# Optimization experiments

Hardware: AMD Instinct MI355X
Metric: run time of the kernel (lower is better)

The kernel has to match this reference:

```python
import jax, jax.numpy as jnp
import numpy as np

N_HEADS = 12
EMBED_DIM = 768
QKV_DIM = 64


def setup_inputs() -> dict:
    key = jax.random.key(0)
    ks = jax.random.split(key, 6)
    x = jax.random.normal(ks[0], (32, 577, EMBED_DIM), dtype=jnp.float32)
    # per-head Linear weights, torch layout [out, in] stacked over heads: [H, D, E]
    s = 1.0 / np.sqrt(EMBED_DIM)
    wq = jax.random.uniform(ks[1], (N_HEADS, QKV_DIM, EMBED_DIM), jnp.float32, -s, s)
    wk = jax.random.uniform(ks[2], (N_HEADS, QKV_DIM, EMBED_DIM), jnp.float32, -s, s)
    wv = jax.random.uniform(ks[3], (N_HEADS, QKV_DIM, EMBED_DIM), jnp.float32, -s, s)
    sp = 1.0 / np.sqrt(N_HEADS * QKV_DIM)
    w_proj = jax.random.uniform(ks[4], (EMBED_DIM, N_HEADS * QKV_DIM), jnp.float32, -sp, sp)
    b_proj = jax.random.uniform(ks[5], (EMBED_DIM,), jnp.float32, -sp, sp)
    return {"x": x, "wq": wq, "wk": wk, "wv": wv, "w_proj": w_proj, "b_proj": b_proj}


def reference(x, wq, wk, wv, w_proj, b_proj):
    scale = QKV_DIM ** (-0.5)
    # batched per-head projections: x [B,S,E], w* [H,D,E] -> [B,H,S,D]
    q = jnp.einsum('bse,hde->bhsd', x, wq)
    k = jnp.einsum('bse,hde->bhsd', x, wk)
    v = jnp.einsum('bse,hde->bhsd', x, wv)
    scores = jnp.einsum('bhsd,bhtd->bhst', q, k) * scale  # [B,H,S,S]
    attn = jax.nn.softmax(scores, axis=-1)
    out = jnp.einsum('bhst,bhtd->bhsd', attn, v)          # [B,H,S,D]
    # concat heads in head order along last dim: [B,S,H*D]
    B, H, S, D = out.shape
    cat = jnp.transpose(out, (0, 2, 1, 3)).reshape(B, S, H * D)
    return cat @ w_proj.T + b_proj
```

## Files before the change

### kernel.cpp

```cpp
#include <hip/hip_runtime.h>

#define TOK    18464
#define SEQ    577
#define EMB    768
#define NH     12
#define HD     64
#define HEADSZ 36928
#define PLANE  14180352
#define SPAD   640

typedef float f32x4 __attribute__((ext_vector_type(4)));
typedef short s16x8 __attribute__((ext_vector_type(8)));

__device__ __forceinline__ unsigned short f2bf(float f) {
  unsigned u = __builtin_bit_cast(unsigned, f);
  return (unsigned short)((u + 0x7fffu + ((u >> 16) & 1u)) >> 16);
}
__device__ __forceinline__ unsigned pk2bf(float a, float b) {
  return (unsigned)f2bf(a) | ((unsigned)f2bf(b) << 16);
}
__device__ __forceinline__ float fexp2(float x) {
  float r; asm("v_exp_f32 %0, %1" : "=v"(r) : "v"(x)); return r;
}

__device__ __forceinline__ void gload16(const void* g, void* l) {
  __builtin_amdgcn_global_load_lds(
      (const __attribute__((address_space(1))) void*)g,
      (__attribute__((address_space(3))) void*)l, 16, 0, 0);
}

__global__ void cvt_x(const float* __restrict__ src, short* __restrict__ dst, int n8) {
  int i = blockIdx.x * blockDim.x + threadIdx.x;
  if (i >= n8) return;
  const float4* s4 = reinterpret_cast<const float4*>(src + (size_t)i * 8);
  float4 a = s4[0], b = s4[1];
  s16x8 o;
  o[0] = (short)f2bf(a.x); o[1] = (short)f2bf(a.y);
  o[2] = (short)f2bf(a.z); o[3] = (short)f2bf(a.w);
  o[4] = (short)f2bf(b.x); o[5] = (short)f2bf(b.y);
  o[6] = (short)f2bf(b.z); o[7] = (short)f2bf(b.w);
  *reinterpret_cast<s16x8*>(dst + (size_t)i * 8) = o;
}

__global__ void cvt_w(const float* __restrict__ wq, const float* __restrict__ wk,
                      const float* __restrict__ wv, const float* __restrict__ wp,
                      short* __restrict__ wqkv, short* __restrict__ wpb) {
  int tid = blockIdx.x * blockDim.x + threadIdx.x;
  if (tid >= 294912) return;
  int region = tid / 73728;
  int off = (tid % 73728) * 8;
  const float* s; short* d;
  if (region == 0)      { s = wq + off; d = wqkv + off; }
  else if (region == 1) { s = wk + off; d = wqkv + 589824 + off; }
  else if (region == 2) { s = wv + off; d = wqkv + 2 * 589824 + off; }
  else                  { s = wp + off; d = wpb + off; }
  const float4* s4 = reinterpret_cast<const float4*>(s);
  float4 a = s4[0], b = s4[1];
  s16x8 o;
  o[0] = (short)f2bf(a.x); o[1] = (short)f2bf(a.y);
  o[2] = (short)f2bf(a.z); o[3] = (short)f2bf(a.w);
  o[4] = (short)f2bf(b.x); o[5] = (short)f2bf(b.y);
  o[6] = (short)f2bf(b.z); o[7] = (short)f2bf(b.w);
  *reinterpret_cast<s16x8*>(d) = o;
}

template <int MODE>
__launch_bounds__(256)
__global__ void gemm_bt(const short* __restrict__ A, const short* __restrict__ Bw,
                        short* __restrict__ qk_out, short* __restrict__ vt_out,
                        float* __restrict__ out, const float* __restrict__ bias,
                        int M, int nnt) {
  __shared__ short As[128 * 32];
  __shared__ short Bs[128 * 32];
  int bid = blockIdx.x, nwg = gridDim.x;
  int qq = nwg >> 3, rr = nwg & 7;
  int xcd = bid & 7, loc = bid >> 3;
  int wgid = (xcd < rr ? xcd * (qq + 1) : rr * (qq + 1) + (xcd - rr) * qq) + loc;
  int tn = wgid % nnt;
  int tm = wgid / nnt;
  int tid = threadIdx.x;
  int w = tid >> 6, lane = tid & 63;
  int wm = w >> 1, wn = w & 1;
  int lr = lane & 15, lg = lane >> 4;
  int m0 = tm * 128, n0 = tn * 128;

  f32x4 acc[4][4] = {};

  int srow = tid >> 2;
  int scol = (tid & 3) * 8;

  for (int kt = 0; kt < 24; ++kt) {
    int kb = kt * 32;
    __syncthreads();
    #pragma unroll
    for (int it = 0; it < 2; ++it) {
      int row = srow + it * 64;
      int gr = m0 + row; if (gr >= M) gr = M - 1;
      gload16(A + (size_t)gr * EMB + kb + scol, (char*)As + w * 1024 + it * 4096);
      int rb = n0 + row;
      gload16(Bw + (size_t)rb * EMB + kb + scol, (char*)Bs + w * 1024 + it * 4096);
    }
    __syncthreads();
    s16x8 af[4], bfr[4];
    #pragma unroll
    for (int f = 0; f < 4; ++f) {
      af[f]  = *reinterpret_cast<const s16x8*>(&As[(wm * 64 + f * 16 + lr) * 32 + lg * 8]);
      bfr[f] = *reinterpret_cast<const s16x8*>(&Bs[(wn * 64 + f * 16 + lr) * 32 + lg * 8]);
    }
    #pragma unroll
    for (int i = 0; i < 4; ++i)
      #pragma unroll
      for (int j = 0; j < 4; ++j)
        acc[i][j] = __builtin_amdgcn_mfma_f32_16x16x32_bf16(af[i], bfr[j], acc[i][j], 0, 0, 0);
  }

  int mbase = m0 + wm * 64;
  int nbase = n0 + wn * 64;
  #pragma unroll
  for (int i = 0; i < 4; ++i) {
    #pragma unroll
    for (int j = 0; j < 4; ++j) {
      #pragma unroll
      for (int r = 0; r < 4; ++r) {
        int row = mbase + i * 16 + lg * 4 + r;
        int col = nbase + j * 16 + lr;
        if (row < M) {
          float v = acc[i][j][r];
          if (MODE == 0) {
            int b = row / SEQ;
            int s = row - b * SEQ;
            if (col >= 1536) {
              int rem = col - 1536;
              int h = rem >> 6, d = rem & 63;
              vt_out[((size_t)(b * NH + h) * HD + d) * SPAD + s] = (short)f2bf(v);
            } else {
              int which = (col >= 768) ? 1 : 0;
              int rem = col - which * 768;
              int h = rem >> 6, d = rem & 63;
              qk_out[(size_t)which * PLANE + ((size_t)b * NH + h) * HEADSZ + s * HD + d] =
                  (short)f2bf(v);
            }
          } else {
            out[(size_t)row * EMB + col] = v + bias[col];
          }
        }
      }
    }
  }
}

__launch_bounds__(256)
__global__ void attn(const short* __restrict__ qkv, const short* __restrict__ vt,
                     short* __restrict__ cat) {
  int bid = blockIdx.x;
  int wgid = (bid & 7) * 240 + (bid >> 3);
  int bh = wgid / 5, qt = wgid % 5;
  int b = bh / NH, h = bh % NH;
  const short* Q   = qkv + (size_t)bh * HEADSZ;
  const char* KpB  = (const char*)(qkv + (size_t)PLANE + (size_t)bh * HEADSZ);
  const char* VtpB = (const char*)(vt + (size_t)bh * (HD * SPAD));

  __shared__ char KVs[16384];
  __shared__ short Pl[4][32 * 72];

  int tid = threadIdx.x, w = tid >> 6, lane = tid & 63;
  int lr = lane & 15, lg = lane >> 4;
  int q0 = qt * 128;
  short* Pw = &Pl[w][0];

  s16x8 qf[2][2];
  #pragma unroll
  for (int rb = 0; rb < 2; ++rb) {
    int row = q0 + w * 32 + rb * 16 + lr; if (row >= SEQ) row = SEQ - 1;
    #pragma unroll
    for (int kk = 0; kk < 2; ++kk)
      qf[rb][kk] = *reinterpret_cast<const s16x8*>(&Q[row * HD + kk * 32 + lg * 8]);
  }

  int srow0 = tid >> 3;
  int scb   = (tid & 7) * 16;
  int swz  = (lr & 7) << 4;
  int ka0  = lr * 128 + ((lg * 16) ^ swz);

  f32x4 acco[2][4] = {};
  float lsum[2] = {0.f, 0.f};
  const float SCL = 0.18033688f;
  const f32x4 NEG16 = {-16.f, -16.f, -16.f, -16.f};

  for (int tt = 0; tt < 10; ++tt) {
    int t0 = tt * 64;

    __syncthreads();
    #pragma unroll
    for (int it = 0; it < 2; ++it) {
      int row = srow0 + it * 32;
      int cb  = scb ^ ((row & 7) << 4);
      int ldst = row * 128 + scb;
      int grow = t0 + row; if (grow > 576) grow = 576;
      gload16(KpB + (size_t)grow * 128 + cb, KVs + ldst);
      gload16(VtpB + (size_t)row * (SPAD * 2) + t0 * 2 + cb, KVs + 8192 + ldst);
    }
    __syncthreads();

    #pragma unroll
    for (int fk = 0; fk < 4; ++fk) {
      s16x8 kf0 = *reinterpret_cast<const s16x8*>(KVs + fk * 2048 + ka0);
      s16x8 kf1 = *reinterpret_cast<const s16x8*>(KVs + fk * 2048 + (ka0 ^ 64));
      f32x4 s0 = NEG16, s1 = NEG16;
      s0 = __builtin_amdgcn_mfma_f32_16x16x32_bf16(kf0, qf[0][0], s0, 0, 0, 0);
      s0 = __builtin_amdgcn_mfma_f32_16x16x32_bf16(kf1, qf[0][1], s0, 0, 0, 0);
      s1 = __builtin_amdgcn_mfma_f32_16x16x32_bf16(kf0, qf[1][0], s1, 0, 0, 0);
      s1 = __builtin_amdgcn_mfma_f32_16x16x32_bf16(kf1, qf[1][1], s1, 0, 0, 0);
      #pragma unroll
      for (int r = 0; r < 4; ++r) {
        bool ok = (t0 + fk * 16 + lg * 4 + r) < SEQ;
        s0[r] = ok ? s0[r] * SCL : -1e30f;
        s1[r] = ok ? s1[r] * SCL : -1e30f;
      }
      {
        float p0 = fexp2(s0[0]), p1 = fexp2(s0[1]);
        float p2 = fexp2(s0[2]), p3 = fexp2(s0[3]);
        lsum[0] += (p0 + p1) + (p2 + p3);
        uint2 pk; pk.x = pk2bf(p0, p1); pk.y = pk2bf(p2, p3);
        *reinterpret_cast<uint2*>(&Pw[(size_t)lr * 72 + fk * 16 + lg * 4]) = pk;
      }
      {
        float p0 = fexp2(s1[0]), p1 = fexp2(s1[1]);
        float p2 = fexp2(s1[2]), p3 = fexp2(s1[3]);
        lsum[1] += (p0 + p1) + (p2 + p3);
        uint2 pk; pk.x = pk2bf(p0, p1); pk.y = pk2bf(p2, p3);
        *reinterpret_cast<uint2*>(&Pw[(size_t)(16 + lr) * 72 + fk * 16 + lg * 4]) = pk;
      }
    }

    s16x8 pf[2][2];
    #pragma unroll
    for (int rb = 0; rb < 2; ++rb)
      #pragma unroll
      for (int kk = 0; kk < 2; ++kk)
        pf[rb][kk] = *reinterpret_cast<const s16x8*>(&Pw[(rb * 16 + lr) * 72 + kk * 32 + lg * 8]);

    #pragma unroll
    for (int f = 0; f < 4; ++f) {
      s16x8 vf0 = *reinterpret_cast<const s16x8*>(KVs + 8192 + f * 2048 + ka0);
      s16x8 vf1 = *reinterpret_cast<const s16x8*>(KVs + 8192 + f * 2048 + (ka0 ^ 64));
      acco[0][f] = __builtin_amdgcn_mfma_f32_16x16x32_bf16(pf[0][0], vf0, acco[0][f], 0, 0, 0);
      acco[0][f] = __builtin_amdgcn_mfma_f32_16x16x32_bf16(pf[0][1], vf1, acco[0][f], 0, 0, 0);
      acco[1][f] = __builtin_amdgcn_mfma_f32_16x16x32_bf16(pf[1][0], vf0, acco[1][f], 0, 0, 0);
      acco[1][f] = __builtin_amdgcn_mfma_f32_16x16x32_bf16(pf[1][1], vf1, acco[1][f], 0, 0, 0);
    }
  }

  #pragma unroll
  for (int rb = 0; rb < 2; ++rb) {
    lsum[rb] += __shfl_xor(lsum[rb], 16);
    lsum[rb] += __shfl_xor(lsum[rb], 32);
  }

  #pragma unroll
  for (int rb = 0; rb < 2; ++rb) {
    #pragma unroll
    for (int r = 0; r < 4; ++r) {
      float li = __shfl(lsum[rb], lg * 4 + r);
      int s = q0 + w * 32 + rb * 16 + lg * 4 + r;
      if (s < SEQ) {
        float inv = 1.0f / li;
        #pragma unroll
        for (int f = 0; f < 4; ++f)
          cat[((size_t)b * SEQ + s) * EMB + h * HD + f * 16 + lr] =
              (short)f2bf(acco[rb][f][r] * inv);
      }
    }
  }
}

extern "C" void kernel_launch(void* const* d_in, const int* in_sizes, int n_in,
                              void* d_out, int out_size, void* d_ws, size_t ws_size,
                              hipStream_t stream) {
  const float* x  = (const float*)d_in[0];
  const float* wq = (const float*)d_in[1];
  const float* wk = (const float*)d_in[2];
  const float* wv = (const float*)d_in[3];
  const float* wp = (const float*)d_in[4];
  const float* bp = (const float*)d_in[5];
  float* out = (float*)d_out;

  char* ws = (char*)d_ws;
  short* xb   = (short*)ws;
  short* wqkv = (short*)(ws + 28360704);
  short* wpb  = (short*)(ws + 31899648);
  short* qkb  = (short*)(ws + 33079296);
  short* vtb  = (short*)(ws + 89800704);
  short* cat  = xb;

  hipMemsetAsync(vtb, 0, 31457280, stream);
  cvt_x<<<6924, 256, 0, stream>>>(x, xb, 1772544);
  cvt_w<<<1152, 256, 0, stream>>>(wq, wk, wv, wp, wqkv, wpb);
  gemm_bt<0><<<145 * 18, 256, 0, stream>>>(xb, wqkv, qkb, vtb, nullptr, nullptr, TOK, 18);
  attn<<<1920, 256, 0, stream>>>(qkb, vtb, cat);
  gemm_bt<1><<<145 * 6, 256, 0, stream>>>(cat, wpb, nullptr, nullptr, out, bp, TOK, 6);
}
```

Baseline: 273.1 us.

## Double-buffer LDS tiles in GEMM and attention to overlap loads with MFMA

Adds two-stage LDS double buffering to both the bf16 GEMM and the attention kernel. The next K-slice (or K/V tile) is prefetched into the alternate buffer with direct-to-LDS loads while MFMAs run on the current one, and each iteration now needs one barrier instead of two. The goal is to hide global load latency. In exchange LDS use doubles (32 KB for the GEMM, about 50 KB for attention), which may reduce occupancy. Correctness relies on gload16 completing before the trailing barrier, so the change depends on the compiler inserting the right vmcnt waits.

```diff
diff --git a/kernel.cpp b/kernel.cpp
--- a/kernel.cpp
+++ b/kernel.cpp
@@ -70,8 +70,8 @@
                         short* __restrict__ qk_out, short* __restrict__ vt_out,
                         float* __restrict__ out, const float* __restrict__ bias,
                         int M, int nnt) {
-  __shared__ short As[128 * 32];
-  __shared__ short Bs[128 * 32];
+  __shared__ short As[2][128 * 32];
+  __shared__ short Bs[2][128 * 32];
   int bid = blockIdx.x, nwg = gridDim.x;
   int qq = nwg >> 3, rr = nwg & 7;
   int xcd = bid & 7, loc = bid >> 3;
@@ -89,30 +89,41 @@
   int srow = tid >> 2;
   int scol = (tid & 3) * 8;
 
+#define G_STAGE(buf, kt)                                                          \
+  {                                                                               \
+    int kb = (kt) * 32;                                                           \
+    _Pragma("unroll")                                                             \
+    for (int it = 0; it < 2; ++it) {                                              \
+      int row = srow + it * 64;                                                   \
+      int gr = m0 + row; if (gr >= M) gr = M - 1;                                 \
+      gload16(A + (size_t)gr * EMB + kb + scol, (char*)As[buf] + w * 1024 + it * 4096); \
+      int rb = n0 + row;                                                          \
+      gload16(Bw + (size_t)rb * EMB + kb + scol, (char*)Bs[buf] + w * 1024 + it * 4096); \
+    }                                                                             \
+  }
+
+  G_STAGE(0, 0);
+  __syncthreads();
+
   for (int kt = 0; kt < 24; ++kt) {
-    int kb = kt * 32;
-    __syncthreads();
-    #pragma unroll
-    for (int it = 0; it < 2; ++it) {
-      int row = srow + it * 64;
-      int gr = m0 + row; if (gr >= M) gr = M - 1;
-      gload16(A + (size_t)gr * EMB + kb + scol, (char*)As + w * 1024 + it * 4096);
-      int rb = n0 + row;
-      gload16(Bw + (size_t)rb * EMB + kb + scol, (char*)Bs + w * 1024 + it * 4096);
-    }
-    __syncthreads();
+    int cur = kt & 1;
+    if (kt < 23) G_STAGE(cur ^ 1, kt + 1);
+
     s16x8 af[4], bfr[4];
     #pragma unroll
     for (int f = 0; f < 4; ++f) {
-      af[f]  = *reinterpret_cast<const s16x8*>(&As[(wm * 64 + f * 16 + lr) * 32 + lg * 8]);
-      bfr[f] = *reinterpret_cast<const s16x8*>(&Bs[(wn * 64 + f * 16 + lr) * 32 + lg * 8]);
+      af[f]  = *reinterpret_cast<const s16x8*>(&As[cur][(wm * 64 + f * 16 + lr) * 32 + lg * 8]);
+      bfr[f] = *reinterpret_cast<const s16x8*>(&Bs[cur][(wn * 64 + f * 16 + lr) * 32 + lg * 8]);
     }
     #pragma unroll
     for (int i = 0; i < 4; ++i)
       #pragma unroll
       for (int j = 0; j < 4; ++j)
         acc[i][j] = __builtin_amdgcn_mfma_f32_16x16x32_bf16(af[i], bfr[j], acc[i][j], 0, 0, 0);
-  }
+
+    __syncthreads();
+  }
+#undef G_STAGE
 
   int mbase = m0 + wm * 64;
   int nbase = n0 + wn * 64;
@@ -160,7 +171,7 @@
   const char* KpB  = (const char*)(qkv + (size_t)PLANE + (size_t)bh * HEADSZ);
   const char* VtpB = (const char*)(vt + (size_t)bh * (HD * SPAD));
 
-  __shared__ char KVs[16384];
+  __shared__ char KVs[2][16384];
   __shared__ short Pl[4][32 * 72];
 
   int tid = threadIdx.x, w = tid >> 6, lane = tid & 63;
@@ -187,25 +198,34 @@
   const float SCL = 0.18033688f;
   const f32x4 NEG16 = {-16.f, -16.f, -16.f, -16.f};
 
+#define KV_STAGE(buf, t0s)                                                        \
+  {                                                                               \
+    _Pragma("unroll")                                                             \
+    for (int it = 0; it < 2; ++it) {                                              \
+      int row = srow0 + it * 32;                                                  \
+      int cb  = scb ^ ((row & 7) << 4);                                           \
+      int ldst = row * 128 + scb;                                                 \
+      int grow = (t0s) + row; if (grow > 576) grow = 576;                         \
+      gload16(KpB + (size_t)grow * 128 + cb, KVs[buf] + ldst);                    \
+      gload16(VtpB + (size_t)row * (SPAD * 2) + (t0s) * 2 + cb, KVs[buf] + 8192 + ldst); \
+    }                                                                             \
+  }
+
+  KV_STAGE(0, 0);
+  __syncthreads();
+
   for (int tt = 0; tt < 10; ++tt) {
     int t0 = tt * 64;
-
-    __syncthreads();
-    #pragma unroll
-    for (int it = 0; it < 2; ++it) {
-      int row = srow0 + it * 32;
-      int cb  = scb ^ ((row & 7) << 4);
-      int ldst = row * 128 + scb;
-      int grow = t0 + row; if (grow > 576) grow = 576;
-      gload16(KpB + (size_t)grow * 128 + cb, KVs + ldst);
-      gload16(VtpB + (size_t)row * (SPAD * 2) + t0 * 2 + cb, KVs + 8192 + ldst);
-    }
-    __syncthreads();
+    int cur = tt & 1;
+    if (tt < 9) KV_STAGE(cur ^ 1, t0 + 64);
+
+    const char* Ks = KVs[cur];
+    const char* Vs = KVs[cur] + 8192;
 
     #pragma unroll
     for (int fk = 0; fk < 4; ++fk) {
-      s16x8 kf0 = *reinterpret_cast<const s16x8*>(KVs + fk * 2048 + ka0);
-      s16x8 kf1 = *reinterpret_cast<const s16x8*>(KVs + fk * 2048 + (ka0 ^ 64));
+      s16x8 kf0 = *reinterpret_cast<const s16x8*>(Ks + fk * 2048 + ka0);
+      s16x8 kf1 = *reinterpret_cast<const s16x8*>(Ks + fk * 2048 + (ka0 ^ 64));
       f32x4 s0 = NEG16, s1 = NEG16;
       s0 = __builtin_amdgcn_mfma_f32_16x16x32_bf16(kf0, qf[0][0], s0, 0, 0, 0);
       s0 = __builtin_amdgcn_mfma_f32_16x16x32_bf16(kf1, qf[0][1], s0, 0, 0, 0);
@@ -242,14 +262,17 @@
 
     #pragma unroll
     for (int f = 0; f < 4; ++f) {
-      s16x8 vf0 = *reinterpret_cast<const s16x8*>(KVs + 8192 + f * 2048 + ka0);
-      s16x8 vf1 = *reinterpret_cast<const s16x8*>(KVs + 8192 + f * 2048 + (ka0 ^ 64));
+      s16x8 vf0 = *reinterpret_cast<const s16x8*>(Vs + f * 2048 + ka0);
+      s16x8 vf1 = *reinterpret_cast<const s16x8*>(Vs + f * 2048 + (ka0 ^ 64));
       acco[0][f] = __builtin_amdgcn_mfma_f32_16x16x32_bf16(pf[0][0], vf0, acco[0][f], 0, 0, 0);
       acco[0][f] = __builtin_amdgcn_mfma_f32_16x16x32_bf16(pf[0][1], vf1, acco[0][f], 0, 0, 0);
       acco[1][f] = __builtin_amdgcn_mfma_f32_16x16x32_bf16(pf[1][0], vf0, acco[1][f], 0, 0, 0);
       acco[1][f] = __builtin_amdgcn_mfma_f32_16x16x32_bf16(pf[1][1], vf1, acco[1][f], 0, 0, 0);
     }
-  }
+
+    __syncthreads();
+  }
+#undef KV_STAGE
 
   #pragma unroll
   for (int rb = 0; rb < 2; ++rb) {
```

Measured after the change: 279.7 us. 2.4% more time.
